# Kernel optimization log

Measured on AMD Instinct MI355X. Metric: run time of the kernel, lower is better.

The kernel has to match this reference:

```python
import jax, jax.numpy as jnp
import numpy as np

# multi-scale pyramid (low2high: lowest resolution first), d_model etc. from module defaults
SHAPES = ((8, 8), (16, 16), (32, 32), (64, 64))
D, HEADS, DH, PTS, NLV, NLAYERS, DFF = 256, 8, 32, 4, 4, 6, 1024
L_TOTAL = sum(h * w for h, w in SHAPES)  # 5440
B = 4


def _ref_points():
    # normalized (x, y) pixel centers per level, concatenated -> [L_TOTAL, 2]
    pts = []
    for (H, W) in SHAPES:
        ry = (jnp.arange(H, dtype=jnp.float32) + 0.5) / H
        rx = (jnp.arange(W, dtype=jnp.float32) + 0.5) / W
        gy, gx = jnp.meshgrid(ry, rx, indexing='ij')
        pts.append(jnp.stack([gx.ravel(), gy.ravel()], -1))
    return jnp.concatenate(pts, 0)


def _lev_ids():
    return jnp.concatenate([jnp.full((h * w,), l, dtype=jnp.int32)
                            for l, (h, w) in enumerate(SHAPES)])


def _layer_norm(x, g, b):
    m = jnp.mean(x, -1, keepdims=True)
    v = jnp.mean((x - m) ** 2, -1, keepdims=True)
    return g * (x - m) * jax.lax.rsqrt(v + 1e-5) + b


def _ms_deform_attn(q, src, ref, w_off, b_off, w_attn, b_attn, w_val, b_val, w_out, b_out):
    Bq, L, _ = q.shape
    v = (src @ w_val + b_val).reshape(Bq, L, HEADS, DH)
    off = (q @ w_off + b_off).reshape(Bq, L, HEADS, NLV, PTS, 2)
    aw = jax.nn.softmax((q @ w_attn + b_attn).reshape(Bq, L, HEADS, NLV * PTS), -1)
    aw = aw.reshape(Bq, L, HEADS, NLV, PTS)
    # offset normalizer is (W, H) per level
    norm = jnp.array([[w, h] for (h, w) in SHAPES], dtype=q.dtype)
    loc = ref[None, :, None, None, None, :] + off / norm[None, None, None, :, None, :]
    out = jnp.zeros((Bq, L, HEADS, DH), q.dtype)
    start = 0
    for l, (H_, W_) in enumerate(SHAPES):
        vl = v[:, start:start + H_ * W_].transpose(0, 2, 1, 3)  # [B, heads, HW, dh]
        # grid_sample(align_corners=False): pixel coord = loc * size - 0.5
        x = loc[:, :, :, l, :, 0] * W_ - 0.5  # [B, L, heads, P]
        y = loc[:, :, :, l, :, 1] * H_ - 0.5
        x0 = jnp.floor(x).astype(jnp.int32)
        y0 = jnp.floor(y).astype(jnp.int32)
        fx = x - x0
        fy = y - y0

        def corner(ix, iy, w):
            inb = ((ix >= 0) & (ix < W_) & (iy >= 0) & (iy < H_)).astype(q.dtype)
            idx = jnp.clip(iy, 0, H_ - 1) * W_ + jnp.clip(ix, 0, W_ - 1)
            idx = idx.transpose(0, 2, 1, 3).reshape(Bq, HEADS, L * PTS, 1)
            g = jnp.take_along_axis(vl, idx, axis=2)  # [B, heads, L*P, dh]
            wt = (w * inb).transpose(0, 2, 1, 3).reshape(Bq, HEADS, L * PTS, 1)
            return g * wt

        samp = (corner(x0, y0, (1 - fx) * (1 - fy))
                + corner(x0 + 1, y0, fx * (1 - fy))
                + corner(x0, y0 + 1, (1 - fx) * fy)
                + corner(x0 + 1, y0 + 1, fx * fy))
        samp = samp.reshape(Bq, HEADS, L, PTS, DH)
        out = out + jnp.einsum('blhp,bhlpd->blhd', aw[:, :, :, l, :], samp)
        start += H_ * W_
    return out.reshape(Bq, L, D) @ w_out + b_out


def setup_inputs() -> dict:
    key = jax.random.key(0)
    ks = jax.random.split(key, 16)
    s = 0.02
    inp = {
        'src': jax.random.normal(ks[0], (B, L_TOTAL, D), jnp.float32),
        'pos': jax.random.normal(ks[1], (B, L_TOTAL, D), jnp.float32),
        'level_embed': jax.random.normal(ks[2], (NLV, D), jnp.float32),
        'w_off': jax.random.normal(ks[3], (NLAYERS, D, HEADS * NLV * PTS * 2), jnp.float32) * s,
        'b_off': jnp.zeros((NLAYERS, HEADS * NLV * PTS * 2), jnp.float32),
        'w_attn': jax.random.normal(ks[4], (NLAYERS, D, HEADS * NLV * PTS), jnp.float32) * s,
        'b_attn': jnp.zeros((NLAYERS, HEADS * NLV * PTS), jnp.float32),
        'w_val': jax.random.normal(ks[5], (NLAYERS, D, D), jnp.float32) * s,
        'b_val': jnp.zeros((NLAYERS, D), jnp.float32),
        'w_out': jax.random.normal(ks[6], (NLAYERS, D, D), jnp.float32) * s,
        'b_out': jnp.zeros((NLAYERS, D), jnp.float32),
        'ln1_g': jnp.ones((NLAYERS, D), jnp.float32),
        'ln1_b': jnp.zeros((NLAYERS, D), jnp.float32),
        'w_ff1': jax.random.normal(ks[7], (NLAYERS, D, DFF), jnp.float32) * s,
        'b_ff1': jnp.zeros((NLAYERS, DFF), jnp.float32),
        'w_ff2': jax.random.normal(ks[8], (NLAYERS, DFF, D), jnp.float32) * s,
        'b_ff2': jnp.zeros((NLAYERS, D), jnp.float32),
        'ln2_g': jnp.ones((NLAYERS, D), jnp.float32),
        'ln2_b': jnp.zeros((NLAYERS, D), jnp.float32),
    }
    return inp


def reference(src, pos, level_embed, w_off, b_off, w_attn, b_attn, w_val, b_val,
              w_out, b_out, ln1_g, ln1_b, w_ff1, b_ff1, w_ff2, b_ff2, ln2_g, ln2_b):
    # lvl_pos_embed = pos + level_embed[level-of-token] (masks all False -> valid_ratios == 1)
    lvl_pos = pos + level_embed[_lev_ids()]
    ref = _ref_points().astype(src.dtype)
    x = src
    for i in range(NLAYERS):
        q = x + lvl_pos
        x2 = _ms_deform_attn(q, x, ref, w_off[i], b_off[i], w_attn[i], b_attn[i],
                             w_val[i], b_val[i], w_out[i], b_out[i])
        x = _layer_norm(x + x2, ln1_g[i], ln1_b[i])
        ff = jax.nn.relu(x @ w_ff1[i] + b_ff1[i]) @ w_ff2[i] + b_ff2[i]
        x = _layer_norm(x + ff, ln2_g[i], ln2_b[i])
    return x
```

## Files before the change

kernel.cpp:

```cpp
#include <hip/hip_runtime.h>

#define LTOT 5440
#define NTOK 21760

typedef float  f32x4  __attribute__((ext_vector_type(4)));
typedef float  f32x2  __attribute__((ext_vector_type(2)));
typedef short  short8 __attribute__((ext_vector_type(8)));

__device__ __forceinline__ unsigned short f2bf(float f) {
  unsigned int u = __float_as_uint(f);
  u += 0x7FFF + ((u >> 16) & 1);
  return (unsigned short)(u >> 16);
}
__device__ __forceinline__ float bf2f(unsigned short u) {
  return __uint_as_float(((unsigned int)u) << 16);
}

__global__ void wconv(const float* __restrict__ w_off, const float* __restrict__ w_attn,
                      const float* __restrict__ w_val, const float* __restrict__ w_out,
                      const float* __restrict__ w_ff1, const float* __restrict__ w_ff2,
                      unsigned short* __restrict__ dst) {
  int tid = blockIdx.x * 256 + threadIdx.x;
  const int PER = 753664;
  if (tid >= 6 * PER) return;
  int layer = tid / PER;
  int rem = tid - layer * PER;
  int base, K, N;
  const float* src;
  if (rem < 65536)       { base = 0;      K = 256;  N = 256;  src = w_off; }
  else if (rem < 98304)  { base = 65536;  K = 256;  N = 128;  src = w_attn; }
  else if (rem < 163840) { base = 98304;  K = 256;  N = 256;  src = w_val; }
  else if (rem < 229376) { base = 163840; K = 256;  N = 256;  src = w_out; }
  else if (rem < 491520) { base = 229376; K = 256;  N = 1024; src = w_ff1; }
  else                   { base = 491520; K = 1024; N = 256;  src = w_ff2; }
  int local = rem - base;
  int n = local / K, k = local - n * K;
  dst[tid] = f2bf(src[(size_t)layer * K * N + (size_t)k * N + n]);
}

__global__ void bpack(const float* __restrict__ b_off, const float* __restrict__ b_attn,
                      float* __restrict__ fb) {
  int l = blockIdx.x, t = threadIdx.x;
  fb[l * 384 + t] = (t < 256) ? b_off[l * 256 + t] : b_attn[l * 128 + t - 256];
}

__global__ void prep(const float* __restrict__ src, const float* __restrict__ pos,
                     const float* __restrict__ lev_emb, float* __restrict__ x,
                     unsigned short* __restrict__ xb, unsigned short* __restrict__ qb) {
  int i = blockIdx.x * 256 + threadIdx.x;
  int d4 = i & 63;
  int tok = (i >> 6) % LTOT;
  int lev = (tok < 64) ? 0 : (tok < 320) ? 1 : (tok < 1344) ? 2 : 3;
  float4 s = ((const float4*)src)[i];
  float4 pv = ((const float4*)pos)[i];
  float4 lv = ((const float4*)lev_emb)[lev * 64 + d4];
  ((float4*)x)[i] = s;
  ushort4 o;
  o.x = f2bf(s.x); o.y = f2bf(s.y); o.z = f2bf(s.z); o.w = f2bf(s.w);
  ((ushort4*)xb)[i] = o;
  ushort4 q;
  q.x = f2bf(s.x + pv.x + lv.x);
  q.y = f2bf(s.y + pv.y + lv.y);
  q.z = f2bf(s.z + pv.z + lv.z);
  q.w = f2bf(s.w + pv.w + lv.w);
  ((ushort4*)qb)[i] = q;
}

template<bool RELU, bool OBF16>
__global__ __launch_bounds__(256) void gemm_tn(
    const unsigned short* __restrict__ A, const unsigned short* __restrict__ Wt,
    const float* __restrict__ bias, void* __restrict__ Cout,
    int M, int N, int K) {
  __shared__ __align__(16) unsigned short a_lds[128 * 64];
  __shared__ __align__(16) unsigned short b_lds[128 * 64];
  int m0 = blockIdx.x * 128;
  int n0 = blockIdx.y * 128;
  int t = threadIdx.x;
  int w = t >> 6, l = t & 63;
  int wr = (w >> 1) * 64, wc = (w & 1) * 64;
  int lr = l & 15, lk = (l >> 4) * 8;

  f32x4 acc[4][4] = {};

  for (int k0 = 0; k0 < K; k0 += 64) {
#pragma unroll
    for (int i = 0; i < 4; ++i) {
      int c = i * 256 + t;
      int row = c >> 3, off8 = (c & 7) * 8;
      const unsigned short* gp = A + (size_t)(m0 + row) * K + k0 + off8;
      __builtin_amdgcn_global_load_lds(
          (const __attribute__((address_space(1))) void*)gp,
          (__attribute__((address_space(3))) void*)(a_lds + c * 8), 16, 0, 0);
    }
#pragma unroll
    for (int i = 0; i < 4; ++i) {
      int c = i * 256 + t;
      int row = c >> 3, off8 = (c & 7) * 8;
      const unsigned short* gp = Wt + (size_t)(n0 + row) * K + k0 + off8;
      __builtin_amdgcn_global_load_lds(
          (const __attribute__((address_space(1))) void*)gp,
          (__attribute__((address_space(3))) void*)(b_lds + c * 8), 16, 0, 0);
    }
    __syncthreads();
#pragma unroll
    for (int kk = 0; kk < 64; kk += 32) {
      short8 af[4], bfr[4];
#pragma unroll
      for (int m = 0; m < 4; ++m)
        af[m] = *(const short8*)(a_lds + (wr + m * 16 + lr) * 64 + kk + lk);
#pragma unroll
      for (int n = 0; n < 4; ++n)
        bfr[n] = *(const short8*)(b_lds + (wc + n * 16 + lr) * 64 + kk + lk);
#pragma unroll
      for (int m = 0; m < 4; ++m)
#pragma unroll
        for (int n = 0; n < 4; ++n)
          acc[m][n] = __builtin_amdgcn_mfma_f32_16x16x32_bf16(af[m], bfr[n], acc[m][n], 0, 0, 0);
    }
    __syncthreads();
  }

  int rb = (l >> 4) * 4;
#pragma unroll
  for (int n = 0; n < 4; ++n) {
    int col = n0 + wc + n * 16 + lr;
    float bv = bias[col];
#pragma unroll
    for (int m = 0; m < 4; ++m) {
#pragma unroll
      for (int r = 0; r < 4; ++r) {
        int row = m0 + wr + m * 16 + rb + r;
        float v = acc[m][n][r] + bv;
        if (RELU) v = fmaxf(v, 0.0f);
        if (OBF16) ((unsigned short*)Cout)[(size_t)row * N + col] = f2bf(v);
        else       ((float*)Cout)[(size_t)row * N + col] = v;
      }
    }
  }
}

__global__ __launch_bounds__(256) void ms_sample(
    const float* __restrict__ offattn, const unsigned short* __restrict__ vb,
    unsigned short* __restrict__ samp) {
  __shared__ __align__(16) uint2 sWI[512];
  int bid = blockIdx.x;
  int bl = (bid & 7) * (NTOK / 8) + (bid >> 3);
  int t = threadIdx.x;
  int l = bl % LTOT;
  int bbase = (bl - l) * 256;
  if (t < 128) {
    float logit = offattn[(size_t)bl * 384 + 256 + t];
    float mx = logit;
#pragma unroll
    for (int o = 1; o < 16; o <<= 1) mx = fmaxf(mx, __shfl_xor(mx, o));
    float e = __expf(logit - mx);
    float ssum = e;
#pragma unroll
    for (int o = 1; o < 16; o <<= 1) ssum += __shfl_xor(ssum, o);
    float aw = e / ssum;

    int lev = (t >> 2) & 3;
    int lev_q = (l < 64) ? 0 : (l < 320) ? 1 : (l < 1344) ? 2 : 3;
    int start_q = (lev_q == 0) ? 0 : (lev_q == 1) ? 64 : (lev_q == 2) ? 320 : 1344;
    int shq = lev_q + 3;
    int r = l - start_q;
    int Wq = 1 << shq;
    int iy = r >> shq, ix = r & (Wq - 1);
    float invWq = 1.0f / (float)Wq;
    float refx = ((float)ix + 0.5f) * invWq;
    float refy = ((float)iy + 0.5f) * invWq;
    int iW = 8 << lev;
    float Wl = (float)iW;
    int start_l = (lev == 0) ? 0 : (lev == 1) ? 64 : (lev == 2) ? 320 : 1344;
    float ox = offattn[(size_t)bl * 384 + 2 * t];
    float oy = offattn[(size_t)bl * 384 + 2 * t + 1];
    float gx = refx * Wl + ox - 0.5f;
    float gy = refy * Wl + oy - 0.5f;
    float flx = floorf(gx), fly = floorf(gy);
    int x0 = (int)flx, y0 = (int)fly;
    float fx = gx - flx, fy = gy - fly;
#pragma unroll
    for (int c = 0; c < 4; ++c) {
      int cx = x0 + (c & 1);
      int cy = y0 + (c >> 1);
      int inb = (cx >= 0) && (cx < iW) && (cy >= 0) && (cy < iW);
      int cxc = cx < 0 ? 0 : (cx > iW - 1 ? iW - 1 : cx);
      int cyc = cy < 0 ? 0 : (cy > iW - 1 ? iW - 1 : cy);
      float wx = (c & 1) ? fx : 1.0f - fx;
      float wy = (c & 2) ? fy : 1.0f - fy;
      float wgt = inb ? aw * wx * wy : 0.0f;
      unsigned int idxb = (unsigned int)(start_l + cyc * iW + cxc) * 512u;
      sWI[t * 4 + c] = make_uint2(__float_as_uint(wgt), idxb);
    }
  }
  __syncthreads();
  int h = t >> 5, j = t & 31;
  int q = j >> 3, p = j & 7;
  int rotp = ((h & 1) << 2) | q;
  const uint2* wiBase = sWI + h * 64 + q * 16;
  unsigned int chb = (unsigned int)(h * 32 + p * 4) * 2u;
  const char* vB = (const char*)(vb + bbase);
  f32x2 a01 = {0.0f, 0.0f}, a23 = {0.0f, 0.0f};
#pragma unroll
  for (int kp = 0; kp < 8; ++kp) {
    int kq = ((kp + rotp) & 7) * 2;
    uint4 wi2 = *(const uint4*)(wiBase + kq);
    float w0 = __uint_as_float(wi2.x);
    float w1 = __uint_as_float(wi2.z);
    uint2 u0 = *(const uint2*)(vB + (wi2.y + chb));
    uint2 u1 = *(const uint2*)(vB + (wi2.w + chb));
    f32x2 v01a = { __uint_as_float(u0.x << 16), __uint_as_float(u0.x & 0xffff0000u) };
    f32x2 v23a = { __uint_as_float(u0.y << 16), __uint_as_float(u0.y & 0xffff0000u) };
    f32x2 w0v = {w0, w0};
    a01 = __builtin_elementwise_fma(w0v, v01a, a01);
    a23 = __builtin_elementwise_fma(w0v, v23a, a23);
    f32x2 v01b = { __uint_as_float(u1.x << 16), __uint_as_float(u1.x & 0xffff0000u) };
    f32x2 v23b = { __uint_as_float(u1.y << 16), __uint_as_float(u1.y & 0xffff0000u) };
    f32x2 w1v = {w1, w1};
    a01 = __builtin_elementwise_fma(w1v, v01b, a01);
    a23 = __builtin_elementwise_fma(w1v, v23b, a23);
  }
  float c0 = a01.x, c1 = a01.y, c2 = a23.x, c3 = a23.y;
  c0 += __shfl_xor(c0, 8);  c1 += __shfl_xor(c1, 8);
  c2 += __shfl_xor(c2, 8);  c3 += __shfl_xor(c3, 8);
  c0 += __shfl_xor(c0, 16); c1 += __shfl_xor(c1, 16);
  c2 += __shfl_xor(c2, 16); c3 += __shfl_xor(c3, 16);
  if (q == 0) {
    uint2 pk;
    pk.x = (unsigned int)f2bf(c0) | ((unsigned int)f2bf(c1) << 16);
    pk.y = (unsigned int)f2bf(c2) | ((unsigned int)f2bf(c3) << 16);
    *(uint2*)(samp + (size_t)bl * 256 + h * 32 + p * 4) = pk;
  }
}

template<bool QADD>
__global__ __launch_bounds__(256) void ln_fused(
    const float* __restrict__ xin, const float* __restrict__ yin,
    const float* __restrict__ g, const float* __restrict__ bb,
    const float* __restrict__ pos, const float* __restrict__ lev_emb,
    float* __restrict__ xout, unsigned short* __restrict__ xbout,
    unsigned short* __restrict__ qbout) {
  int row = blockIdx.x * 4 + (threadIdx.x >> 6);
  int lane = threadIdx.x & 63;
  size_t base = (size_t)row * 64 + lane;
  float4 xv = ((const float4*)xin)[base];
  float4 yv = ((const float4*)yin)[base];
  float4 tv;
  tv.x = xv.x + yv.x; tv.y = xv.y + yv.y; tv.z = xv.z + yv.z; tv.w = xv.w + yv.w;
  float s = tv.x + tv.y + tv.z + tv.w;
  float s2 = tv.x * tv.x + tv.y * tv.y + tv.z * tv.z + tv.w * tv.w;
#pragma unroll
  for (int o = 1; o < 64; o <<= 1) {
    s += __shfl_xor(s, o, 64);
    s2 += __shfl_xor(s2, o, 64);
  }
  float mean = s * (1.0f / 256.0f);
  float var = s2 * (1.0f / 256.0f) - mean * mean;
  float rstd = rsqrtf(var + 1e-5f);
  float4 gv = ((const float4*)g)[lane];
  float4 bv = ((const float4*)bb)[lane];
  float4 o;
  o.x = gv.x * (tv.x - mean) * rstd + bv.x;
  o.y = gv.y * (tv.y - mean) * rstd + bv.y;
  o.z = gv.z * (tv.z - mean) * rstd + bv.z;
  o.w = gv.w * (tv.w - mean) * rstd + bv.w;
  ((float4*)xout)[base] = o;
  ushort4 ob;
  ob.x = f2bf(o.x); ob.y = f2bf(o.y); ob.z = f2bf(o.z); ob.w = f2bf(o.w);
  ((ushort4*)xbout)[base] = ob;
  if (QADD) {
    int tok = row % LTOT;
    int lev = (tok < 64) ? 0 : (tok < 320) ? 1 : (tok < 1344) ? 2 : 3;
    float4 pv = ((const float4*)pos)[base];
    float4 lv = ((const float4*)lev_emb)[lev * 64 + lane];
    ushort4 q;
    q.x = f2bf(o.x + pv.x + lv.x);
    q.y = f2bf(o.y + pv.y + lv.y);
    q.z = f2bf(o.z + pv.z + lv.z);
    q.w = f2bf(o.w + pv.w + lv.w);
    ((ushort4*)qbout)[base] = q;
  }
}

extern "C" void kernel_launch(void* const* d_in, const int* in_sizes, int n_in,
                              void* d_out, int out_size, void* d_ws, size_t ws_size,
                              hipStream_t stream) {
  (void)in_sizes; (void)n_in; (void)out_size; (void)ws_size;
  const float* src     = (const float*)d_in[0];
  const float* pos     = (const float*)d_in[1];
  const float* lev_emb = (const float*)d_in[2];
  const float* w_off   = (const float*)d_in[3];
  const float* b_off   = (const float*)d_in[4];
  const float* w_attn  = (const float*)d_in[5];
  const float* b_attn  = (const float*)d_in[6];
  const float* w_val   = (const float*)d_in[7];
  const float* b_val   = (const float*)d_in[8];
  const float* w_out   = (const float*)d_in[9];
  const float* b_out   = (const float*)d_in[10];
  const float* ln1_g   = (const float*)d_in[11];
  const float* ln1_b   = (const float*)d_in[12];
  const float* w_ff1   = (const float*)d_in[13];
  const float* b_ff1   = (const float*)d_in[14];
  const float* w_ff2   = (const float*)d_in[15];
  const float* b_ff2   = (const float*)d_in[16];
  const float* ln2_g   = (const float*)d_in[17];
  const float* ln2_b   = (const float*)d_in[18];

  char* ws = (char*)d_ws;
  float*          x     = (float*)(ws + 0);
  float*          y     = (float*)(ws + 22282240);
  unsigned short* xb    = (unsigned short*)(ws + 44564480);
  unsigned short* qb    = (unsigned short*)(ws + 55705600);
  unsigned short* sampb = (unsigned short*)(ws + 55705600);
  float*          offat = (float*)(ws + 66846720);
  unsigned short* vb    = (unsigned short*)(ws + 100270080);
  unsigned short* h1    = (unsigned short*)(ws + 66846720);
  unsigned short* wT    = (unsigned short*)(ws + 111411200);
  float*          fb    = (float*)(ws + 120455168);

  wconv<<<17664, 256, 0, stream>>>(w_off, w_attn, w_val, w_out, w_ff1, w_ff2, wT);
  bpack<<<6, 384, 0, stream>>>(b_off, b_attn, fb);
  prep<<<5440, 256, 0, stream>>>(src, pos, lev_emb, x, xb, qb);

  for (int i = 0; i < 6; ++i) {
    const unsigned short* wl = wT + (size_t)i * 753664;
    gemm_tn<false, false><<<dim3(170, 3), 256, 0, stream>>>(qb, wl + 0,      fb + i * 384,     (void*)offat, NTOK, 384, 256);
    gemm_tn<false, true ><<<dim3(170, 2), 256, 0, stream>>>(xb, wl + 98304,  b_val + i * 256,  (void*)vb,    NTOK, 256, 256);
    ms_sample<<<NTOK, 256, 0, stream>>>(offat, vb, sampb);
    gemm_tn<false, false><<<dim3(170, 2), 256, 0, stream>>>(sampb, wl + 163840, b_out + i * 256, (void*)y,   NTOK, 256, 256);
    ln_fused<false><<<5440, 256, 0, stream>>>(x, y, ln1_g + i * 256, ln1_b + i * 256, pos, lev_emb, x, xb, qb);
    gemm_tn<true,  true ><<<dim3(170, 8), 256, 0, stream>>>(xb, wl + 229376, b_ff1 + i * 1024, (void*)h1,    NTOK, 1024, 256);
    gemm_tn<false, false><<<dim3(170, 2), 256, 0, stream>>>(h1, wl + 491520, b_ff2 + i * 256,  (void*)y,     NTOK, 256, 1024);
    float* xo = (i == 5) ? (float*)d_out : x;
    if (i < 5)
      ln_fused<true ><<<5440, 256, 0, stream>>>(x, y, ln2_g + i * 256, ln2_b + i * 256, pos, lev_emb, xo, xb, qb);
    else
      ln_fused<false><<<5440, 256, 0, stream>>>(x, y, ln2_g + i * 256, ln2_b + i * 256, pos, lev_emb, xo, xb, qb);
  }
}
```

Before: 1.205 ms.

## Fuse residual LayerNorm into output and FF2 GEMM epilogues; batch sampler gathers

Adds a gemm_ln kernel where each block computes a full 256-wide row tile, adds bias and residual, and performs LayerNorm with a cross-wave LDS reduction, writing x, its bf16 copy and the query input directly. This removes the intermediate fp32 y buffer and the separate LN launches. The sampler kernel now loads all weight/index pairs, then issues all value gathers, then accumulates, to increase outstanding memory requests. The fused GEMM uses a larger LDS tile and no pipelining, which may reduce occupancy.

```diff
diff --git a/kernel.cpp b/kernel.cpp
--- a/kernel.cpp
+++ b/kernel.cpp
@@ -11,9 +11,6 @@
   unsigned int u = __float_as_uint(f);
   u += 0x7FFF + ((u >> 16) & 1);
   return (unsigned short)(u >> 16);
-}
-__device__ __forceinline__ float bf2f(unsigned short u) {
-  return __uint_as_float(((unsigned int)u) << 16);
 }
 
 __global__ void wconv(const float* __restrict__ w_off, const float* __restrict__ w_attn,
@@ -139,6 +136,146 @@
   }
 }
 
+template<bool QADD>
+__global__ __launch_bounds__(256) void gemm_ln(
+    const unsigned short* __restrict__ A, const unsigned short* __restrict__ Wt,
+    const float* __restrict__ bias, const float* __restrict__ xres,
+    const float* __restrict__ g, const float* __restrict__ bb,
+    const float* __restrict__ pos, const float* __restrict__ lev_emb,
+    float* __restrict__ xout, unsigned short* __restrict__ xbout,
+    unsigned short* __restrict__ qbout, int K) {
+  __shared__ __align__(16) unsigned short a_lds[64 * 64];
+  __shared__ __align__(16) unsigned short b_lds[256 * 64];
+  __shared__ f32x2 red[64][4];
+  __shared__ f32x2 mr[64];
+  int m0 = blockIdx.x * 64;
+  int t = threadIdx.x;
+  int w = t >> 6, l = t & 63;
+  int wc = w * 64;
+  int lr = l & 15, lk = (l >> 4) * 8;
+
+  f32x4 acc[4][4] = {};
+
+  for (int k0 = 0; k0 < K; k0 += 64) {
+#pragma unroll
+    for (int i = 0; i < 2; ++i) {
+      int c = i * 256 + t;
+      int row = c >> 3, off8 = (c & 7) * 8;
+      const unsigned short* gp = A + (size_t)(m0 + row) * K + k0 + off8;
+      __builtin_amdgcn_global_load_lds(
+          (const __attribute__((address_space(1))) void*)gp,
+          (__attribute__((address_space(3))) void*)(a_lds + c * 8), 16, 0, 0);
+    }
+#pragma unroll
+    for (int i = 0; i < 8; ++i) {
+      int c = i * 256 + t;
+      int row = c >> 3, off8 = (c & 7) * 8;
+      const unsigned short* gp = Wt + (size_t)row * K + k0 + off8;
+      __builtin_amdgcn_global_load_lds(
+          (const __attribute__((address_space(1))) void*)gp,
+          (__attribute__((address_space(3))) void*)(b_lds + c * 8), 16, 0, 0);
+    }
+    __syncthreads();
+#pragma unroll
+    for (int kk = 0; kk < 64; kk += 32) {
+      short8 af[4], bfr[4];
+#pragma unroll
+      for (int m = 0; m < 4; ++m)
+        af[m] = *(const short8*)(a_lds + (m * 16 + lr) * 64 + kk + lk);
+#pragma unroll
+      for (int n = 0; n < 4; ++n)
+        bfr[n] = *(const short8*)(b_lds + (wc + n * 16 + lr) * 64 + kk + lk);
+#pragma unroll
+      for (int m = 0; m < 4; ++m)
+#pragma unroll
+        for (int n = 0; n < 4; ++n)
+          acc[m][n] = __builtin_amdgcn_mfma_f32_16x16x32_bf16(bfr[n], af[m], acc[m][n], 0, 0, 0);
+    }
+    __syncthreads();
+  }
+
+  int rb = (l >> 4) * 4;
+  float4 bv[4];
+#pragma unroll
+  for (int n = 0; n < 4; ++n) bv[n] = *(const float4*)(bias + wc + n * 16 + rb);
+
+  float s[4], s2[4];
+#pragma unroll
+  for (int m = 0; m < 4; ++m) {
+    s[m] = 0.0f; s2[m] = 0.0f;
+    size_t rbase = (size_t)(m0 + m * 16 + lr) * 256;
+#pragma unroll
+    for (int n = 0; n < 4; ++n) {
+      float4 xv = *(const float4*)(xres + rbase + wc + n * 16 + rb);
+      f32x4 v = acc[m][n];
+      v[0] += bv[n].x + xv.x;
+      v[1] += bv[n].y + xv.y;
+      v[2] += bv[n].z + xv.z;
+      v[3] += bv[n].w + xv.w;
+      acc[m][n] = v;
+      s[m]  += v[0] + v[1] + v[2] + v[3];
+      s2[m] += v[0]*v[0] + v[1]*v[1] + v[2]*v[2] + v[3]*v[3];
+    }
+  }
+#pragma unroll
+  for (int m = 0; m < 4; ++m) {
+    s[m]  += __shfl_xor(s[m], 16);  s[m]  += __shfl_xor(s[m], 32);
+    s2[m] += __shfl_xor(s2[m], 16); s2[m] += __shfl_xor(s2[m], 32);
+  }
+  if ((l >> 4) == 0) {
+#pragma unroll
+    for (int m = 0; m < 4; ++m) red[m * 16 + lr][w] = f32x2{s[m], s2[m]};
+  }
+  __syncthreads();
+  if (t < 64) {
+    f32x2 a = red[t][0];
+    f32x2 b2 = red[t][1];
+    f32x2 c2 = red[t][2];
+    f32x2 d2 = red[t][3];
+    float sum = a.x + b2.x + c2.x + d2.x;
+    float sq  = a.y + b2.y + c2.y + d2.y;
+    float mean = sum * (1.0f / 256.0f);
+    float var = sq * (1.0f / 256.0f) - mean * mean;
+    mr[t] = f32x2{mean, rsqrtf(var + 1e-5f)};
+  }
+  __syncthreads();
+
+#pragma unroll
+  for (int m = 0; m < 4; ++m) {
+    f32x2 MR = mr[m * 16 + lr];
+    int row = m0 + m * 16 + lr;
+    size_t rbase = (size_t)row * 256;
+    int tok = row % LTOT;
+    int lev = (tok < 64) ? 0 : (tok < 320) ? 1 : (tok < 1344) ? 2 : 3;
+#pragma unroll
+    for (int n = 0; n < 4; ++n) {
+      int colb = wc + n * 16 + rb;
+      float4 gv  = *(const float4*)(g + colb);
+      float4 bbv = *(const float4*)(bb + colb);
+      f32x4 v = acc[m][n];
+      float4 o;
+      o.x = gv.x * (v[0] - MR.x) * MR.y + bbv.x;
+      o.y = gv.y * (v[1] - MR.x) * MR.y + bbv.y;
+      o.z = gv.z * (v[2] - MR.x) * MR.y + bbv.z;
+      o.w = gv.w * (v[3] - MR.x) * MR.y + bbv.w;
+      *(float4*)(xout + rbase + colb) = o;
+      ushort4 ob;
+      ob.x = f2bf(o.x); ob.y = f2bf(o.y); ob.z = f2bf(o.z); ob.w = f2bf(o.w);
+      *(ushort4*)(xbout + rbase + colb) = ob;
+      if (QADD) {
+        float4 pv = *(const float4*)(pos + rbase + colb);
+        float4 lv = *(const float4*)(lev_emb + lev * 256 + colb);
+        ushort4 qv;
+        qv.x = f2bf(o.x + pv.x + lv.x);
+        qv.y = f2bf(o.y + pv.y + lv.y);
+        qv.z = f2bf(o.z + pv.z + lv.z);
+        qv.w = f2bf(o.w + pv.w + lv.w);
+        *(ushort4*)(qbout + rbase + colb) = qv;
+      }
+    }
+  }
+}
+
 __global__ __launch_bounds__(256) void ms_sample(
     const float* __restrict__ offattn, const unsigned short* __restrict__ vb,
     unsigned short* __restrict__ samp) {
@@ -200,25 +337,32 @@
   const uint2* wiBase = sWI + h * 64 + q * 16;
   unsigned int chb = (unsigned int)(h * 32 + p * 4) * 2u;
   const char* vB = (const char*)(vb + bbase);
-  f32x2 a01 = {0.0f, 0.0f}, a23 = {0.0f, 0.0f};
+  uint4 wi[8];
 #pragma unroll
   for (int kp = 0; kp < 8; ++kp) {
     int kq = ((kp + rotp) & 7) * 2;
-    uint4 wi2 = *(const uint4*)(wiBase + kq);
-    float w0 = __uint_as_float(wi2.x);
-    float w1 = __uint_as_float(wi2.z);
-    uint2 u0 = *(const uint2*)(vB + (wi2.y + chb));
-    uint2 u1 = *(const uint2*)(vB + (wi2.w + chb));
-    f32x2 v01a = { __uint_as_float(u0.x << 16), __uint_as_float(u0.x & 0xffff0000u) };
-    f32x2 v23a = { __uint_as_float(u0.y << 16), __uint_as_float(u0.y & 0xffff0000u) };
-    f32x2 w0v = {w0, w0};
-    a01 = __builtin_elementwise_fma(w0v, v01a, a01);
-    a23 = __builtin_elementwise_fma(w0v, v23a, a23);
-    f32x2 v01b = { __uint_as_float(u1.x << 16), __uint_as_float(u1.x & 0xffff0000u) };
-    f32x2 v23b = { __uint_as_float(u1.y << 16), __uint_as_float(u1.y & 0xffff0000u) };
-    f32x2 w1v = {w1, w1};
-    a01 = __builtin_elementwise_fma(w1v, v01b, a01);
-    a23 = __builtin_elementwise_fma(w1v, v23b, a23);
+    wi[kp] = *(const uint4*)(wiBase + kq);
+  }
+  uint2 u0[8], u1[8];
+#pragma unroll
+  for (int kp = 0; kp < 8; ++kp) {
+    u0[kp] = *(const uint2*)(vB + (wi[kp].y + chb));
+    u1[kp] = *(const uint2*)(vB + (wi[kp].w + chb));
+  }
+  f32x2 a01 = {0.0f, 0.0f}, a23 = {0.0f, 0.0f};
+#pragma unroll
+  for (int kp = 0; kp < 8; ++kp) {
+    float w0 = __uint_as_float(wi[kp].x);
+    float w1 = __uint_as_float(wi[kp].z);
+    f32x2 w0v = {w0, w0}, w1v = {w1, w1};
+    f32x2 va = { __uint_as_float(u0[kp].x << 16), __uint_as_float(u0[kp].x & 0xffff0000u) };
+    f32x2 vbv = { __uint_as_float(u0[kp].y << 16), __uint_as_float(u0[kp].y & 0xffff0000u) };
+    a01 = __builtin_elementwise_fma(w0v, va, a01);
+    a23 = __builtin_elementwise_fma(w0v, vbv, a23);
+    f32x2 vc = { __uint_as_float(u1[kp].x << 16), __uint_as_float(u1[kp].x & 0xffff0000u) };
+    f32x2 vd = { __uint_as_float(u1[kp].y << 16), __uint_as_float(u1[kp].y & 0xffff0000u) };
+    a01 = __builtin_elementwise_fma(w1v, vc, a01);
+    a23 = __builtin_elementwise_fma(w1v, vd, a23);
   }
   float c0 = a01.x, c1 = a01.y, c2 = a23.x, c3 = a23.y;
   c0 += __shfl_xor(c0, 8);  c1 += __shfl_xor(c1, 8);
@@ -230,55 +374,6 @@
     pk.x = (unsigned int)f2bf(c0) | ((unsigned int)f2bf(c1) << 16);
     pk.y = (unsigned int)f2bf(c2) | ((unsigned int)f2bf(c3) << 16);
     *(uint2*)(samp + (size_t)bl * 256 + h * 32 + p * 4) = pk;
-  }
-}
-
-template<bool QADD>
-__global__ __launch_bounds__(256) void ln_fused(
-    const float* __restrict__ xin, const float* __restrict__ yin,
-    const float* __restrict__ g, const float* __restrict__ bb,
-    const float* __restrict__ pos, const float* __restrict__ lev_emb,
-    float* __restrict__ xout, unsigned short* __restrict__ xbout,
-    unsigned short* __restrict__ qbout) {
-  int row = blockIdx.x * 4 + (threadIdx.x >> 6);
-  int lane = threadIdx.x & 63;
-  size_t base = (size_t)row * 64 + lane;
-  float4 xv = ((const float4*)xin)[base];
-  float4 yv = ((const float4*)yin)[base];
-  float4 tv;
-  tv.x = xv.x + yv.x; tv.y = xv.y + yv.y; tv.z = xv.z + yv.z; tv.w = xv.w + yv.w;
-  float s = tv.x + tv.y + tv.z + tv.w;
-  float s2 = tv.x * tv.x + tv.y * tv.y + tv.z * tv.z + tv.w * tv.w;
-#pragma unroll
-  for (int o = 1; o < 64; o <<= 1) {
-    s += __shfl_xor(s, o, 64);
-    s2 += __shfl_xor(s2, o, 64);
-  }
-  float mean = s * (1.0f / 256.0f);
-  float var = s2 * (1.0f / 256.0f) - mean * mean;
-  float rstd = rsqrtf(var + 1e-5f);
-  float4 gv = ((const float4*)g)[lane];
-  float4 bv = ((const float4*)bb)[lane];
-  float4 o;
-  o.x = gv.x * (tv.x - mean) * rstd + bv.x;
-  o.y = gv.y * (tv.y - mean) * rstd + bv.y;
-  o.z = gv.z * (tv.z - mean) * rstd + bv.z;
-  o.w = gv.w * (tv.w - mean) * rstd + bv.w;
-  ((float4*)xout)[base] = o;
-  ushort4 ob;
-  ob.x = f2bf(o.x); ob.y = f2bf(o.y); ob.z = f2bf(o.z); ob.w = f2bf(o.w);
-  ((ushort4*)xbout)[base] = ob;
-  if (QADD) {
-    int tok = row % LTOT;
-    int lev = (tok < 64) ? 0 : (tok < 320) ? 1 : (tok < 1344) ? 2 : 3;
-    float4 pv = ((const float4*)pos)[base];
-    float4 lv = ((const float4*)lev_emb)[lev * 64 + lane];
-    ushort4 q;
-    q.x = f2bf(o.x + pv.x + lv.x);
-    q.y = f2bf(o.y + pv.y + lv.y);
-    q.z = f2bf(o.z + pv.z + lv.z);
-    q.w = f2bf(o.w + pv.w + lv.w);
-    ((ushort4*)qbout)[base] = q;
   }
 }
 
@@ -308,7 +403,6 @@
 
   char* ws = (char*)d_ws;
   float*          x     = (float*)(ws + 0);
-  float*          y     = (float*)(ws + 22282240);
   unsigned short* xb    = (unsigned short*)(ws + 44564480);
   unsigned short* qb    = (unsigned short*)(ws + 55705600);
   unsigned short* sampb = (unsigned short*)(ws + 55705600);
@@ -324,17 +418,21 @@
 
   for (int i = 0; i < 6; ++i) {
     const unsigned short* wl = wT + (size_t)i * 753664;
-    gemm_tn<false, false><<<dim3(170, 3), 256, 0, stream>>>(qb, wl + 0,      fb + i * 384,     (void*)offat, NTOK, 384, 256);
-    gemm_tn<false, true ><<<dim3(170, 2), 256, 0, stream>>>(xb, wl + 98304,  b_val + i * 256,  (void*)vb,    NTOK, 256, 256);
+    gemm_tn<false, false><<<dim3(170, 3), 256, 0, stream>>>(qb, wl + 0,     fb + i * 384,    (void*)offat, NTOK, 384, 256);
+    gemm_tn<false, true ><<<dim3(170, 2), 256, 0, stream>>>(xb, wl + 98304, b_val + i * 256, (void*)vb,    NTOK, 256, 256);
     ms_sample<<<NTOK, 256, 0, stream>>>(offat, vb, sampb);
-    gemm_tn<false, false><<<dim3(170, 2), 256, 0, stream>>>(sampb, wl + 163840, b_out + i * 256, (void*)y,   NTOK, 256, 256);
-    ln_fused<false><<<5440, 256, 0, stream>>>(x, y, ln1_g + i * 256, ln1_b + i * 256, pos, lev_emb, x, xb, qb);
-    gemm_tn<true,  true ><<<dim3(170, 8), 256, 0, stream>>>(xb, wl + 229376, b_ff1 + i * 1024, (void*)h1,    NTOK, 1024, 256);
-    gemm_tn<false, false><<<dim3(170, 2), 256, 0, stream>>>(h1, wl + 491520, b_ff2 + i * 256,  (void*)y,     NTOK, 256, 1024);
+    gemm_ln<false><<<340, 256, 0, stream>>>(sampb, wl + 163840, b_out + i * 256, x,
+                                            ln1_g + i * 256, ln1_b + i * 256,
+                                            pos, lev_emb, x, xb, qb, 256);
+    gemm_tn<true, true ><<<dim3(170, 8), 256, 0, stream>>>(xb, wl + 229376, b_ff1 + i * 1024, (void*)h1, NTOK, 1024, 256);
     float* xo = (i == 5) ? (float*)d_out : x;
     if (i < 5)
-      ln_fused<true ><<<5440, 256, 0, stream>>>(x, y, ln2_g + i * 256, ln2_b + i * 256, pos, lev_emb, xo, xb, qb);
+      gemm_ln<true ><<<340, 256, 0, stream>>>(h1, wl + 491520, b_ff2 + i * 256, x,
+                                              ln2_g + i * 256, ln2_b + i * 256,
+                                              pos, lev_emb, xo, xb, qb, 1024);
     else
-      ln_fused<false><<<5440, 256, 0, stream>>>(x, y, ln2_g + i * 256, ln2_b + i * 256, pos, lev_emb, xo, xb, qb);
-  }
-}
+      gemm_ln<false><<<340, 256, 0, stream>>>(h1, wl + 491520, b_ff2 + i * 256, x,
+                                              ln2_g + i * 256, ln2_b + i * 256,
+                                              pos, lev_emb, xo, xb, qb, 1024);
+  }
+}
```

After: 1.372 ms. 1.14x slower.

## Merge offset/value projection GEMMs, use 64-row tiles for N=256 GEMMs, batch sampler loads

Applied to the files above, without the earlier changes.

Folds the offset/attention and value projection GEMMs into one launch that picks its operands by grid column, removing a kernel launch and giving the GPU more blocks at once. Adds a 64x128 tile GEMM variant for the N=256 output projection and FFN2, doubling the block count from 340 to 680 to fill more compute units. In the deformable sampler, all weight/index reads and value gathers are issued up front before the FMAs so the loads can overlap. The cost is more registers per thread and lower data reuse per block in the smaller-tile GEMM.

```diff
diff --git a/kernel.cpp b/kernel.cpp
--- a/kernel.cpp
+++ b/kernel.cpp
@@ -11,9 +11,6 @@
   unsigned int u = __float_as_uint(f);
   u += 0x7FFF + ((u >> 16) & 1);
   return (unsigned short)(u >> 16);
-}
-__device__ __forceinline__ float bf2f(unsigned short u) {
-  return __uint_as_float(((unsigned int)u) << 16);
 }
 
 __global__ void wconv(const float* __restrict__ w_off, const float* __restrict__ w_attn,
@@ -139,6 +136,158 @@
   }
 }
 
+template<bool RELU, bool OBF16>
+__global__ __launch_bounds__(256) void gemm_tn64(
+    const unsigned short* __restrict__ A, const unsigned short* __restrict__ Wt,
+    const float* __restrict__ bias, void* __restrict__ Cout,
+    int M, int N, int K) {
+  __shared__ __align__(16) unsigned short a_lds[64 * 64];
+  __shared__ __align__(16) unsigned short b_lds[128 * 64];
+  int m0 = blockIdx.x * 64;
+  int n0 = blockIdx.y * 128;
+  int t = threadIdx.x;
+  int w = t >> 6, l = t & 63;
+  int wr = (w >> 1) * 32, wc = (w & 1) * 64;
+  int lr = l & 15, lk = (l >> 4) * 8;
+
+  f32x4 acc[2][4] = {};
+
+  for (int k0 = 0; k0 < K; k0 += 64) {
+#pragma unroll
+    for (int i = 0; i < 2; ++i) {
+      int c = i * 256 + t;
+      int row = c >> 3, off8 = (c & 7) * 8;
+      const unsigned short* gp = A + (size_t)(m0 + row) * K + k0 + off8;
+      __builtin_amdgcn_global_load_lds(
+          (const __attribute__((address_space(1))) void*)gp,
+          (__attribute__((address_space(3))) void*)(a_lds + c * 8), 16, 0, 0);
+    }
+#pragma unroll
+    for (int i = 0; i < 4; ++i) {
+      int c = i * 256 + t;
+      int row = c >> 3, off8 = (c & 7) * 8;
+      const unsigned short* gp = Wt + (size_t)(n0 + row) * K + k0 + off8;
+      __builtin_amdgcn_global_load_lds(
+          (const __attribute__((address_space(1))) void*)gp,
+          (__attribute__((address_space(3))) void*)(b_lds + c * 8), 16, 0, 0);
+    }
+    __syncthreads();
+#pragma unroll
+    for (int kk = 0; kk < 64; kk += 32) {
+      short8 af[2], bfr[4];
+#pragma unroll
+      for (int m = 0; m < 2; ++m)
+        af[m] = *(const short8*)(a_lds + (wr + m * 16 + lr) * 64 + kk + lk);
+#pragma unroll
+      for (int n = 0; n < 4; ++n)
+        bfr[n] = *(const short8*)(b_lds + (wc + n * 16 + lr) * 64 + kk + lk);
+#pragma unroll
+      for (int m = 0; m < 2; ++m)
+#pragma unroll
+        for (int n = 0; n < 4; ++n)
+          acc[m][n] = __builtin_amdgcn_mfma_f32_16x16x32_bf16(af[m], bfr[n], acc[m][n], 0, 0, 0);
+    }
+    __syncthreads();
+  }
+
+  int rb = (l >> 4) * 4;
+#pragma unroll
+  for (int n = 0; n < 4; ++n) {
+    int col = n0 + wc + n * 16 + lr;
+    float bv = bias[col];
+#pragma unroll
+    for (int m = 0; m < 2; ++m) {
+#pragma unroll
+      for (int r = 0; r < 4; ++r) {
+        int row = m0 + wr + m * 16 + rb + r;
+        float v = acc[m][n][r] + bv;
+        if (RELU) v = fmaxf(v, 0.0f);
+        if (OBF16) ((unsigned short*)Cout)[(size_t)row * N + col] = f2bf(v);
+        else       ((float*)Cout)[(size_t)row * N + col] = v;
+      }
+    }
+  }
+}
+
+__global__ __launch_bounds__(256) void gemm_proj(
+    const unsigned short* __restrict__ qb, const unsigned short* __restrict__ xb,
+    const unsigned short* __restrict__ wOA, const unsigned short* __restrict__ wV,
+    const float* __restrict__ bOA, const float* __restrict__ bV,
+    float* __restrict__ offat, unsigned short* __restrict__ vb) {
+  __shared__ __align__(16) unsigned short a_lds[128 * 64];
+  __shared__ __align__(16) unsigned short b_lds[128 * 64];
+  const int K = 256;
+  int by = blockIdx.y;
+  bool isV = (by >= 3);
+  const unsigned short* A  = isV ? xb : qb;
+  const unsigned short* Wt = isV ? wV : wOA;
+  const float* bias        = isV ? bV : bOA;
+  int N  = isV ? 256 : 384;
+  int n0 = (isV ? (by - 3) : by) * 128;
+  int m0 = blockIdx.x * 128;
+  int t = threadIdx.x;
+  int w = t >> 6, l = t & 63;
+  int wr = (w >> 1) * 64, wc = (w & 1) * 64;
+  int lr = l & 15, lk = (l >> 4) * 8;
+
+  f32x4 acc[4][4] = {};
+
+  for (int k0 = 0; k0 < K; k0 += 64) {
+#pragma unroll
+    for (int i = 0; i < 4; ++i) {
+      int c = i * 256 + t;
+      int row = c >> 3, off8 = (c & 7) * 8;
+      const unsigned short* gp = A + (size_t)(m0 + row) * K + k0 + off8;
+      __builtin_amdgcn_global_load_lds(
+          (const __attribute__((address_space(1))) void*)gp,
+          (__attribute__((address_space(3))) void*)(a_lds + c * 8), 16, 0, 0);
+    }
+#pragma unroll
+    for (int i = 0; i < 4; ++i) {
+      int c = i * 256 + t;
+      int row = c >> 3, off8 = (c & 7) * 8;
+      const unsigned short* gp = Wt + (size_t)(n0 + row) * K + k0 + off8;
+      __builtin_amdgcn_global_load_lds(
+          (const __attribute__((address_space(1))) void*)gp,
+          (__attribute__((address_space(3))) void*)(b_lds + c * 8), 16, 0, 0);
+    }
+    __syncthreads();
+#pragma unroll
+    for (int kk = 0; kk < 64; kk += 32) {
+      short8 af[4], bfr[4];
+#pragma unroll
+      for (int m = 0; m < 4; ++m)
+        af[m] = *(const short8*)(a_lds + (wr + m * 16 + lr) * 64 + kk + lk);
+#pragma unroll
+      for (int n = 0; n < 4; ++n)
+        bfr[n] = *(const short8*)(b_lds + (wc + n * 16 + lr) * 64 + kk + lk);
+#pragma unroll
+      for (int m = 0; m < 4; ++m)
+#pragma unroll
+        for (int n = 0; n < 4; ++n)
+          acc[m][n] = __builtin_amdgcn_mfma_f32_16x16x32_bf16(af[m], bfr[n], acc[m][n], 0, 0, 0);
+    }
+    __syncthreads();
+  }
+
+  int rb = (l >> 4) * 4;
+#pragma unroll
+  for (int n = 0; n < 4; ++n) {
+    int col = n0 + wc + n * 16 + lr;
+    float bv = bias[col];
+#pragma unroll
+    for (int m = 0; m < 4; ++m) {
+#pragma unroll
+      for (int r = 0; r < 4; ++r) {
+        int row = m0 + wr + m * 16 + rb + r;
+        float v = acc[m][n][r] + bv;
+        if (isV) vb[(size_t)row * 256 + col] = f2bf(v);
+        else     offat[(size_t)row * 384 + col] = v;
+      }
+    }
+  }
+}
+
 __global__ __launch_bounds__(256) void ms_sample(
     const float* __restrict__ offattn, const unsigned short* __restrict__ vb,
     unsigned short* __restrict__ samp) {
@@ -200,25 +349,32 @@
   const uint2* wiBase = sWI + h * 64 + q * 16;
   unsigned int chb = (unsigned int)(h * 32 + p * 4) * 2u;
   const char* vB = (const char*)(vb + bbase);
-  f32x2 a01 = {0.0f, 0.0f}, a23 = {0.0f, 0.0f};
+  uint4 wi[8];
 #pragma unroll
   for (int kp = 0; kp < 8; ++kp) {
     int kq = ((kp + rotp) & 7) * 2;
-    uint4 wi2 = *(const uint4*)(wiBase + kq);
-    float w0 = __uint_as_float(wi2.x);
-    float w1 = __uint_as_float(wi2.z);
-    uint2 u0 = *(const uint2*)(vB + (wi2.y + chb));
-    uint2 u1 = *(const uint2*)(vB + (wi2.w + chb));
-    f32x2 v01a = { __uint_as_float(u0.x << 16), __uint_as_float(u0.x & 0xffff0000u) };
-    f32x2 v23a = { __uint_as_float(u0.y << 16), __uint_as_float(u0.y & 0xffff0000u) };
-    f32x2 w0v = {w0, w0};
-    a01 = __builtin_elementwise_fma(w0v, v01a, a01);
-    a23 = __builtin_elementwise_fma(w0v, v23a, a23);
-    f32x2 v01b = { __uint_as_float(u1.x << 16), __uint_as_float(u1.x & 0xffff0000u) };
-    f32x2 v23b = { __uint_as_float(u1.y << 16), __uint_as_float(u1.y & 0xffff0000u) };
-    f32x2 w1v = {w1, w1};
-    a01 = __builtin_elementwise_fma(w1v, v01b, a01);
-    a23 = __builtin_elementwise_fma(w1v, v23b, a23);
+    wi[kp] = *(const uint4*)(wiBase + kq);
+  }
+  uint2 u0[8], u1[8];
+#pragma unroll
+  for (int kp = 0; kp < 8; ++kp) {
+    u0[kp] = *(const uint2*)(vB + (wi[kp].y + chb));
+    u1[kp] = *(const uint2*)(vB + (wi[kp].w + chb));
+  }
+  f32x2 a01 = {0.0f, 0.0f}, a23 = {0.0f, 0.0f};
+#pragma unroll
+  for (int kp = 0; kp < 8; ++kp) {
+    float w0 = __uint_as_float(wi[kp].x);
+    float w1 = __uint_as_float(wi[kp].z);
+    f32x2 w0v = {w0, w0}, w1v = {w1, w1};
+    f32x2 va = { __uint_as_float(u0[kp].x << 16), __uint_as_float(u0[kp].x & 0xffff0000u) };
+    f32x2 vbv = { __uint_as_float(u0[kp].y << 16), __uint_as_float(u0[kp].y & 0xffff0000u) };
+    a01 = __builtin_elementwise_fma(w0v, va, a01);
+    a23 = __builtin_elementwise_fma(w0v, vbv, a23);
+    f32x2 vc = { __uint_as_float(u1[kp].x << 16), __uint_as_float(u1[kp].x & 0xffff0000u) };
+    f32x2 vd = { __uint_as_float(u1[kp].y << 16), __uint_as_float(u1[kp].y & 0xffff0000u) };
+    a01 = __builtin_elementwise_fma(w1v, vc, a01);
+    a23 = __builtin_elementwise_fma(w1v, vd, a23);
   }
   float c0 = a01.x, c1 = a01.y, c2 = a23.x, c3 = a23.y;
   c0 += __shfl_xor(c0, 8);  c1 += __shfl_xor(c1, 8);
@@ -324,13 +480,14 @@
 
   for (int i = 0; i < 6; ++i) {
     const unsigned short* wl = wT + (size_t)i * 753664;
-    gemm_tn<false, false><<<dim3(170, 3), 256, 0, stream>>>(qb, wl + 0,      fb + i * 384,     (void*)offat, NTOK, 384, 256);
-    gemm_tn<false, true ><<<dim3(170, 2), 256, 0, stream>>>(xb, wl + 98304,  b_val + i * 256,  (void*)vb,    NTOK, 256, 256);
+    gemm_proj<<<dim3(170, 5), 256, 0, stream>>>(qb, xb, wl + 0, wl + 98304,
+                                                fb + i * 384, b_val + i * 256,
+                                                offat, vb);
     ms_sample<<<NTOK, 256, 0, stream>>>(offat, vb, sampb);
-    gemm_tn<false, false><<<dim3(170, 2), 256, 0, stream>>>(sampb, wl + 163840, b_out + i * 256, (void*)y,   NTOK, 256, 256);
+    gemm_tn64<false, false><<<dim3(340, 2), 256, 0, stream>>>(sampb, wl + 163840, b_out + i * 256, (void*)y, NTOK, 256, 256);
     ln_fused<false><<<5440, 256, 0, stream>>>(x, y, ln1_g + i * 256, ln1_b + i * 256, pos, lev_emb, x, xb, qb);
-    gemm_tn<true,  true ><<<dim3(170, 8), 256, 0, stream>>>(xb, wl + 229376, b_ff1 + i * 1024, (void*)h1,    NTOK, 1024, 256);
-    gemm_tn<false, false><<<dim3(170, 2), 256, 0, stream>>>(h1, wl + 491520, b_ff2 + i * 256,  (void*)y,     NTOK, 256, 1024);
+    gemm_tn<true, true ><<<dim3(170, 8), 256, 0, stream>>>(xb, wl + 229376, b_ff1 + i * 1024, (void*)h1, NTOK, 1024, 256);
+    gemm_tn64<false, false><<<dim3(340, 2), 256, 0, stream>>>(h1, wl + 491520, b_ff2 + i * 256, (void*)y, NTOK, 256, 1024);
     float* xo = (i == 5) ? (float*)d_out : x;
     if (i < 5)
       ln_fused<true ><<<5440, 256, 0, stream>>>(x, y, ln2_g + i * 256, ln2_b + i * 256, pos, lev_emb, xo, xb, qb);
```

Measured after the change: 1.201 ms. No clear change (-0.3%).
